# Kernel tuning notes

Measured on AMD Instinct MI355X. Metric: run time of the kernel, lower is better.

## Reference

```python
import jax, jax.numpy as jnp
import numpy as np

ATTN_WINDOW = 7  # attention_window from attn_params; dilation (attention_stride) = 1


def _xavier(key, shape):
    lim = np.sqrt(6.0 / (shape[0] + shape[1]))
    return jax.random.uniform(key, shape, jnp.float32, -lim, lim)


def setup_inputs() -> dict:
    key = jax.random.key(0)
    ks = jax.random.split(key, 8)
    B, Cin, Him, Wim = 4, 3, 112, 112
    Cmid, Cout = 128, 128
    x = jax.random.normal(ks[0], (B, Cin, Him, Wim), jnp.float32)
    conv_w = jax.random.normal(ks[1], (Cmid, Cin, 3, 3), jnp.float32) * 0.1  # OIHW
    conv_b = jnp.zeros((Cmid,), jnp.float32)
    q_w = _xavier(ks[2], (Cmid, Cmid)); q_b = jnp.zeros((Cmid,), jnp.float32)
    k_w = _xavier(ks[3], (Cmid, Cmid)); k_b = jnp.zeros((Cmid,), jnp.float32)
    v_w = _xavier(ks[4], (Cout, Cmid)); v_b = jnp.zeros((Cout,), jnp.float32)
    return {"x": x, "conv_w": conv_w, "conv_b": conv_b,
            "q_w": q_w, "q_b": q_b, "k_w": k_w, "k_b": k_b, "v_w": v_w, "v_b": v_b}


def _neighbor_idx(n, ksz):
    # NATTEN-style neighborhood: centered window, clamped to stay inside the image.
    starts = jnp.clip(jnp.arange(n) - ksz // 2, 0, n - ksz)
    return starts[:, None] + jnp.arange(ksz)[None, :]  # [n, ksz]


def reference(x, conv_w, conv_b, q_w, q_b, k_w, k_b, v_w, v_b):
    # conv stem (3x3, stride 2, pad 1) + ReLU
    f = jax.lax.conv_general_dilated(
        x, conv_w, window_strides=(2, 2), padding=[(1, 1), (1, 1)],
        dimension_numbers=("NCHW", "OIHW", "NCHW"))
    f = jax.nn.relu(f + conv_b[None, :, None, None])
    f = f.transpose(0, 2, 3, 1)  # NHWC  [B,H,W,Cmid]
    # 1x1 convs == per-pixel linear layers
    q = f @ q_w.T + q_b
    k = f @ k_w.T + k_b
    v = f @ v_w.T + v_b
    B, H, W, C = q.shape
    ksz = min(ATTN_WINDOW, H, W)
    ksz -= 1 if ksz % 2 == 0 else 0
    ih = _neighbor_idx(H, ksz)  # [H, ksz]
    iw = _neighbor_idx(W, ksz)  # [W, ksz]
    # gather per-pixel neighborhoods: [B,H,W,ksz,ksz,C]
    kn = k[:, ih[:, None, :, None], iw[None, :, None, :], :]
    vn = v[:, ih[:, None, :, None], iw[None, :, None, :], :]
    scale = C ** -0.5
    logits = jnp.einsum("bhwc,bhwijc->bhwij", q * scale, kn)
    attn = jax.nn.softmax(logits.reshape(B, H, W, -1), axis=-1).reshape(logits.shape)
    out = jnp.einsum("bhwij,bhwijc->bhwc", attn, vn)  # [B,H,W,Cout]
    return out.transpose(0, 3, 1, 2)  # back to NCHW
```

## Files before the change

kernel.cpp:

```cpp
#include <hip/hip_runtime.h>
#include <hip/hip_bf16.h>
#include <math.h>

#define HW 56
#define PPI (HW*HW)
#define NB 4
#define C 128
#define NPIX (NB*PPI)

typedef __attribute__((ext_vector_type(8))) short short8;
typedef __attribute__((ext_vector_type(4))) float f32x4;

__device__ __forceinline__ short bfbits(float v) {
    __hip_bfloat16 hb = __float2bfloat16(v);
    return *reinterpret_cast<short*>(&hb);
}
__device__ __forceinline__ unsigned packbf(float a, float b) {
    return (unsigned)(unsigned short)bfbits(a) | ((unsigned)(unsigned short)bfbits(b) << 16);
}

__global__ __launch_bounds__(256) void prep_kernel(
    const float* __restrict__ cw,
    const float* __restrict__ qw, const float* __restrict__ kw,
    const float* __restrict__ vw,
    __hip_bfloat16* __restrict__ wcf, __hip_bfloat16* __restrict__ wqkv)
{
    int gid = blockIdx.x * 256 + threadIdx.x;
    if (blockIdx.x < 192) {
        int m   = gid >> 14;
        int r   = gid & 16383;
        int col = r >> 7;
        int k   = r & 127;
        const float* W = (m == 0) ? qw : (m == 1) ? kw : vw;
        int kk = k >> 5, hi = (k >> 3) & 3, j = k & 7;
        wqkv[m * 16384 + ((kk * 4 + hi) * 128 + col) * 8 + j] = __float2bfloat16(W[col * 128 + k]);
    } else {
        int idx = gid - 192 * 256;
        int hi = idx >> 10, cout = (idx >> 3) & 127, j = idx & 7;
        int k  = hi * 8 + j;
        float v = (k < 27) ? cw[cout * 27 + k] : 0.f;
        wcf[(hi * 128 + cout) * 8 + j] = __float2bfloat16(v);
    }
}

#define VPITCH 272
#define XPITCH 24
#define XCH    504
#define LPITCH 100

__global__ __launch_bounds__(256, 3) void fused_kernel(
    const float* __restrict__ x, const __hip_bfloat16* __restrict__ wcf,
    const float* __restrict__ cb, const __hip_bfloat16* __restrict__ wqkv,
    const float* __restrict__ qb, const float* __restrict__ kb,
    const float* __restrict__ vb, float* __restrict__ out)
{
    __shared__ __align__(16) short vT[128 * 136];
    __shared__ __align__(16) short poolA[16 * 128];
    __shared__ __align__(16) short f_ch[16 * 128];
    __shared__ __align__(16) short poolB[16 * 136];
    __shared__ __align__(16) float logit_s[16 * LPITCH];
    short* q_lds   = poolA;
    short* k_chunk = poolA;
    short* x_lds   = poolB;
    short* attnW   = poolB;

    int t = threadIdx.x, lane = t & 63, wid = t >> 6;
    int r16 = lane & 15, hi = lane >> 4;

    int bx = blockIdx.x;
    int b  = bx / 196;
    int rr = bx % 196;
    int th = rr / 14, tw = rr % 14;
    int ih0 = min(max(th*4 - 3, 0), HW - 10);
    int iw0 = min(max(tw*4 - 3, 0), HW - 10);

    {
        int ihA = 2*ih0 - 1, iwA = 2*iw0 - 1;
        #pragma unroll
        for (int it = 0; it < 6; ++it) {
            int i = t + 256*it;
            if (i < 1512) {
                int ci = i / XCH, r = i % XCH;
                int row = r / XPITCH, col = r % XPITCH;
                int ih = ihA + row, iw = iwA + col;
                float xv = 0.f;
                if (col < 21 && ih >= 0 && ih < 112 && iw >= 0 && iw < 112)
                    xv = x[((size_t)(b*3 + ci)*112 + ih)*112 + iw];
                x_lds[i] = bfbits(xv);
            }
        }
    }

    for (int i = t; i < 1024; i += 256) {
        int c = i >> 3, j = i & 7;
        int hsw = (c >> 3) & 7;
        int unit = (14 + (j >> 2)) ^ hsw;
        *(unsigned*)((char*)vT + c*VPITCH + (unit << 4) + (j & 3)*4) = 0u;
    }

    int cout0 = (wid*2 + 0)*16 + r16;
    int cout1 = (wid*2 + 1)*16 + r16;
    short8 cbw0 = *(const short8*)((const short*)wcf + (hi*128 + cout0)*8);
    short8 cbw1 = *(const short8*)((const short*)wcf + (hi*128 + cout1)*8);
    float cbias0 = cb[cout0], cbias1 = cb[cout1];

    int  offb[8];
    bool vmask[8];
    #pragma unroll
    for (int j = 0; j < 8; ++j) {
        int k = hi*8 + j;
        int ci = k/9, r9 = k%9, kh = r9/3, kw_ = r9%3;
        offb[j]  = ci*XCH + kh*XPITCH + kw_;
        vmask[j] = (k < 27);
    }

    float kvbias[4];
    #pragma unroll
    for (int i = 0; i < 4; ++i) {
        int idx = wid*4 + i, mv = idx >> 3, ct = idx & 7, c = ct*16 + r16;
        kvbias[i] = mv ? vb[c] : kb[c];
    }
    float qbias[2];
    #pragma unroll
    for (int i = 0; i < 2; ++i) qbias[i] = qb[(wid*2 + i)*16 + r16];

    __syncthreads();

    auto conv_to_fch = [&](int hl, int wl) {
        int pb = hl*(2*XPITCH) + wl*2;
        short8 af;
        #pragma unroll
        for (int j = 0; j < 8; ++j)
            af[j] = vmask[j] ? x_lds[offb[j] + pb] : (short)0;
        #pragma unroll
        for (int ctl = 0; ctl < 2; ++ctl) {
            int cout   = ctl ? cout1  : cout0;
            short8 bw  = ctl ? cbw1   : cbw0;
            float bias = ctl ? cbias1 : cbias0;
            f32x4 acc = {0.f, 0.f, 0.f, 0.f};
            acc = __builtin_amdgcn_mfma_f32_16x16x32_bf16(af, bw, acc, 0, 0, 0);
            int colblk = cout >> 3, inb = (cout & 7)*2;
            #pragma unroll
            for (int rg = 0; rg < 4; ++rg) {
                int px = hi*4 + rg;
                *(short*)((char*)f_ch + px*256 + ((colblk ^ px) << 4) + inb)
                    = bfbits(fmaxf(acc[rg] + bias, 0.f));
            }
        }
    };

    short8 qa[4];
    {
        int ph = th*4 + (r16 >> 2), pw = tw*4 + (r16 & 3);
        conv_to_fch(ph - ih0, pw - iw0);
        __syncthreads();

        short8 fa[4];
        #pragma unroll
        for (int kk = 0; kk < 4; ++kk)
            fa[kk] = *(const short8*)((char*)f_ch + r16*256 + (((kk*4 + hi) ^ r16) << 4));

        #pragma unroll
        for (int i = 0; i < 2; ++i) {
            int ct = wid*2 + i;
            const short* wb = (const short*)wqkv + hi*1024 + r16*8 + ct*128;
            f32x4 acc = {0.f, 0.f, 0.f, 0.f};
            acc = __builtin_amdgcn_mfma_f32_16x16x32_bf16(fa[0], *(const short8*)(wb),         acc, 0, 0, 0);
            acc = __builtin_amdgcn_mfma_f32_16x16x32_bf16(fa[1], *(const short8*)(wb +  4096), acc, 0, 0, 0);
            acc = __builtin_amdgcn_mfma_f32_16x16x32_bf16(fa[2], *(const short8*)(wb +  8192), acc, 0, 0, 0);
            acc = __builtin_amdgcn_mfma_f32_16x16x32_bf16(fa[3], *(const short8*)(wb + 12288), acc, 0, 0, 0);
            int c = ct*16 + r16;
            float bb = qbias[i];
            #pragma unroll
            for (int rg = 0; rg < 4; ++rg) {
                int px = hi*4 + rg;
                *(short*)((char*)q_lds + px*256 + (((c >> 3) ^ px) << 4) + (c & 7)*2)
                    = bfbits(acc[rg] + bb);
            }
        }
        __syncthreads();

        #pragma unroll
        for (int kk = 0; kk < 4; ++kk)
            qa[kk] = *(const short8*)((char*)q_lds + r16*256 + (((kk*4 + hi) ^ r16) << 4));
    }

    for (int cc = 0; cc < 7; ++cc) {
        int nc = min(cc*16 + r16, 99);
        conv_to_fch(nc/10, nc%10);
        __syncthreads();

        short8 fa[4];
        #pragma unroll
        for (int kk = 0; kk < 4; ++kk)
            fa[kk] = *(const short8*)((char*)f_ch + r16*256 + (((kk*4 + hi) ^ r16) << 4));

        #pragma unroll
        for (int i = 0; i < 4; ++i) {
            int idx = wid*4 + i;
            int mv  = idx >> 3;
            int ct  = idx & 7;
            const short* wb = (const short*)wqkv + (1+mv)*16384 + hi*1024 + r16*8 + ct*128;
            f32x4 acc = {0.f, 0.f, 0.f, 0.f};
            acc = __builtin_amdgcn_mfma_f32_16x16x32_bf16(fa[0], *(const short8*)(wb),         acc, 0, 0, 0);
            acc = __builtin_amdgcn_mfma_f32_16x16x32_bf16(fa[1], *(const short8*)(wb +  4096), acc, 0, 0, 0);
            acc = __builtin_amdgcn_mfma_f32_16x16x32_bf16(fa[2], *(const short8*)(wb +  8192), acc, 0, 0, 0);
            acc = __builtin_amdgcn_mfma_f32_16x16x32_bf16(fa[3], *(const short8*)(wb + 12288), acc, 0, 0, 0);
            int c = ct*16 + r16;
            float bb = kvbias[i];
            if (mv == 0) {
                int swz = c >> 3;
                #pragma unroll
                for (int rg = 0; rg < 4; ++rg) {
                    int nl = hi*4 + rg;
                    *(short*)((char*)k_chunk + nl*256 + ((swz ^ nl) << 4) + (c & 7)*2)
                        = bfbits(acc[rg] + bb);
                }
            } else {
                int n0 = cc*16 + hi*4;
                unsigned lo  = packbf(acc[0] + bb, acc[1] + bb);
                unsigned hi2 = packbf(acc[2] + bb, acc[3] + bb);
                int hsw = (c >> 3) & 7;
                int off = (2*n0) ^ (hsw << 4);
                *(uint2*)((char*)vT + c*VPITCH + off) = make_uint2(lo, hi2);
            }
        }
        __syncthreads();

        if ((cc & 3) == wid) {
            const char* kbase = (const char*)k_chunk + r16*256;
            f32x4 acc = {0.f, 0.f, 0.f, 0.f};
            #pragma unroll
            for (int kk = 0; kk < 4; ++kk) {
                short8 kv = *(const short8*)(kbase + (((kk*4 + hi) ^ r16) << 4));
                acc = __builtin_amdgcn_mfma_f32_16x16x32_bf16(qa[kk], kv, acc, 0, 0, 0);
            }
            int col = cc*16 + r16;
            if (col < 100) {
                #pragma unroll
                for (int rg = 0; rg < 4; ++rg)
                    logit_s[(hi*4 + rg)*LPITCH + col] = acc[rg];
            }
        }
    }

    {
        unsigned* aw = (unsigned*)attnW;
        for (int i = t; i < 1088; i += 256) aw[i] = 0u;
    }
    __syncthreads();

    {
        int r7 = lane / 7, s7 = lane - 7*r7;
        bool valid = lane < 49;
        const float scale = 0.08838834764831845f;
        #pragma unroll
        for (int px = 0; px < 4; ++px) {
            int p = wid*4 + px;
            int h = th*4 + (p >> 2), w = tw*4 + (p & 3);
            int hs = min(max(h - 3, 0), HW - 7);
            int ws = min(max(w - 3, 0), HW - 7);
            int col = (hs - ih0 + r7)*10 + (ws - iw0 + s7);
            float lg = valid ? logit_s[p*LPITCH + col] * scale : -INFINITY;
            float m = lg;
            #pragma unroll
            for (int d = 1; d < 64; d <<= 1) m = fmaxf(m, __shfl_xor(m, d));
            float e = valid ? __expf(lg - m) : 0.f;
            float s = e;
            #pragma unroll
            for (int d = 1; d < 64; d <<= 1) s += __shfl_xor(s, d);
            if (valid) {
                __hip_bfloat16 hb = __float2bfloat16(e / s);
                *(__hip_bfloat16*)((char*)attnW + p*VPITCH + 2*col) = hb;
            }
        }
    }
    __syncthreads();

    short8 pa[4];
    #pragma unroll
    for (int kk = 0; kk < 4; ++kk)
        pa[kk] = *(const short8*)((char*)attnW + r16*VPITCH + kk*64 + hi*16);

    for (int nt = wid; nt < 8; nt += 4) {
        int c   = nt*16 + r16;
        int hsw = (c >> 3) & 7;
        const char* vrow = (const char*)vT + c*VPITCH;
        f32x4 acc = {0.f, 0.f, 0.f, 0.f};
        #pragma unroll
        for (int kk = 0; kk < 4; ++kk) {
            short8 vbr = *(const short8*)(vrow + ((kk*64 + hi*16) ^ (hsw << 4)));
            acc = __builtin_amdgcn_mfma_f32_16x16x32_bf16(pa[kk], vbr, acc, 0, 0, 0);
        }
        #pragma unroll
        for (int rg = 0; rg < 4; ++rg) {
            int p = hi*4 + rg;
            int h = th*4 + (p >> 2), w = tw*4 + (p & 3);
            out[(((size_t)b*C + c)*HW + h)*HW + w] = acc[rg];
        }
    }
}

extern "C" void kernel_launch(void* const* d_in, const int* in_sizes, int n_in,
                              void* d_out, int out_size, void* d_ws, size_t ws_size,
                              hipStream_t stream) {
    const float* x      = (const float*)d_in[0];
    const float* conv_w = (const float*)d_in[1];
    const float* conv_b = (const float*)d_in[2];
    const float* q_w    = (const float*)d_in[3];
    const float* q_b    = (const float*)d_in[4];
    const float* k_w    = (const float*)d_in[5];
    const float* k_b    = (const float*)d_in[6];
    const float* v_w    = (const float*)d_in[7];
    const float* v_b    = (const float*)d_in[8];
    float* out = (float*)d_out;

    __hip_bfloat16* wqkv = (__hip_bfloat16*)d_ws;
    __hip_bfloat16* wcf  = wqkv + 3 * 16384;

    prep_kernel<<<208, 256, 0, stream>>>(conv_w, q_w, k_w, v_w, wcf, wqkv);
    fused_kernel<<<NB*196, 256, 0, stream>>>(x, wcf, conv_b, wqkv,
                                             q_b, k_b, v_b, out);
}
```

Before: 45.68 us.

## Give each wave its own neighbor chunk to remove per-chunk block barriers

Instead of all four waves cooperating on each 16-pixel neighbor chunk, with block-wide barriers between the conv, K/V projection and logit stages, each wave now processes whole chunks independently in a private LDS buffer. Only wave-local data dependencies remain, so the seven-iteration loop no longer synchronises. The cost is more registers for per-wave copies of all conv weights and biases, a launch-bounds occupancy drop from 3 to 2 blocks, and load imbalance, since waves 0-2 take two chunks while wave 3 takes one.

```diff
diff --git a/kernel.cpp b/kernel.cpp
--- a/kernel.cpp
+++ b/kernel.cpp
@@ -48,21 +48,19 @@
 #define XCH    504
 #define LPITCH 100
 
-__global__ __launch_bounds__(256, 3) void fused_kernel(
+__global__ __launch_bounds__(256, 2) void fused_kernel(
     const float* __restrict__ x, const __hip_bfloat16* __restrict__ wcf,
     const float* __restrict__ cb, const __hip_bfloat16* __restrict__ wqkv,
     const float* __restrict__ qb, const float* __restrict__ kb,
     const float* __restrict__ vb, float* __restrict__ out)
 {
     __shared__ __align__(16) short vT[128 * 136];
-    __shared__ __align__(16) short poolA[16 * 128];
-    __shared__ __align__(16) short f_ch[16 * 128];
+    __shared__ __align__(16) short poolA[4][16 * 128];
     __shared__ __align__(16) short poolB[16 * 136];
     __shared__ __align__(16) float logit_s[16 * LPITCH];
-    short* q_lds   = poolA;
-    short* k_chunk = poolA;
-    short* x_lds   = poolB;
-    short* attnW   = poolB;
+    short* q_lds = poolA[0];
+    short* x_lds = poolB;
+    short* attnW = poolB;
 
     int t = threadIdx.x, lane = t & 63, wid = t >> 6;
     int r16 = lane & 15, hi = lane >> 4;
@@ -98,12 +96,6 @@
         *(unsigned*)((char*)vT + c*VPITCH + (unit << 4) + (j & 3)*4) = 0u;
     }
 
-    int cout0 = (wid*2 + 0)*16 + r16;
-    int cout1 = (wid*2 + 1)*16 + r16;
-    short8 cbw0 = *(const short8*)((const short*)wcf + (hi*128 + cout0)*8);
-    short8 cbw1 = *(const short8*)((const short*)wcf + (hi*128 + cout1)*8);
-    float cbias0 = cb[cout0], cbias1 = cb[cout1];
-
     int  offb[8];
     bool vmask[8];
     #pragma unroll
@@ -113,20 +105,22 @@
         offb[j]  = ci*XCH + kh*XPITCH + kw_;
         vmask[j] = (k < 27);
     }
-
-    float kvbias[4];
-    #pragma unroll
-    for (int i = 0; i < 4; ++i) {
-        int idx = wid*4 + i, mv = idx >> 3, ct = idx & 7, c = ct*16 + r16;
-        kvbias[i] = mv ? vb[c] : kb[c];
-    }
     float qbias[2];
     #pragma unroll
     for (int i = 0; i < 2; ++i) qbias[i] = qb[(wid*2 + i)*16 + r16];
 
     __syncthreads();
 
-    auto conv_to_fch = [&](int hl, int wl) {
+    short8 qa[4];
+    {
+        int cout0 = (wid*2 + 0)*16 + r16;
+        int cout1 = (wid*2 + 1)*16 + r16;
+        short8 cbw0 = *(const short8*)((const short*)wcf + (hi*128 + cout0)*8);
+        short8 cbw1 = *(const short8*)((const short*)wcf + (hi*128 + cout1)*8);
+        float cbias0 = cb[cout0], cbias1 = cb[cout1];
+
+        int ph = th*4 + (r16 >> 2), pw = tw*4 + (r16 & 3);
+        int hl = ph - ih0, wl = pw - iw0;
         int pb = hl*(2*XPITCH) + wl*2;
         short8 af;
         #pragma unroll
@@ -143,22 +137,18 @@
             #pragma unroll
             for (int rg = 0; rg < 4; ++rg) {
                 int px = hi*4 + rg;
-                *(short*)((char*)f_ch + px*256 + ((colblk ^ px) << 4) + inb)
+                *(short*)((char*)q_lds + px*256 + ((colblk ^ px) << 4) + inb)
                     = bfbits(fmaxf(acc[rg] + bias, 0.f));
             }
         }
-    };
-
-    short8 qa[4];
-    {
-        int ph = th*4 + (r16 >> 2), pw = tw*4 + (r16 & 3);
-        conv_to_fch(ph - ih0, pw - iw0);
         __syncthreads();
 
         short8 fa[4];
         #pragma unroll
         for (int kk = 0; kk < 4; ++kk)
-            fa[kk] = *(const short8*)((char*)f_ch + r16*256 + (((kk*4 + hi) ^ r16) << 4));
+            fa[kk] = *(const short8*)((char*)q_lds + r16*256 + (((kk*4 + hi) ^ r16) << 4));
+
+        __syncthreads();
 
         #pragma unroll
         for (int i = 0; i < 2; ++i) {
@@ -183,66 +173,109 @@
         #pragma unroll
         for (int kk = 0; kk < 4; ++kk)
             qa[kk] = *(const short8*)((char*)q_lds + r16*256 + (((kk*4 + hi) ^ r16) << 4));
-    }
-
-    for (int cc = 0; cc < 7; ++cc) {
-        int nc = min(cc*16 + r16, 99);
-        conv_to_fch(nc/10, nc%10);
         __syncthreads();
-
-        short8 fa[4];
-        #pragma unroll
-        for (int kk = 0; kk < 4; ++kk)
-            fa[kk] = *(const short8*)((char*)f_ch + r16*256 + (((kk*4 + hi) ^ r16) << 4));
-
-        #pragma unroll
-        for (int i = 0; i < 4; ++i) {
-            int idx = wid*4 + i;
-            int mv  = idx >> 3;
-            int ct  = idx & 7;
-            const short* wb = (const short*)wqkv + (1+mv)*16384 + hi*1024 + r16*8 + ct*128;
-            f32x4 acc = {0.f, 0.f, 0.f, 0.f};
-            acc = __builtin_amdgcn_mfma_f32_16x16x32_bf16(fa[0], *(const short8*)(wb),         acc, 0, 0, 0);
-            acc = __builtin_amdgcn_mfma_f32_16x16x32_bf16(fa[1], *(const short8*)(wb +  4096), acc, 0, 0, 0);
-            acc = __builtin_amdgcn_mfma_f32_16x16x32_bf16(fa[2], *(const short8*)(wb +  8192), acc, 0, 0, 0);
-            acc = __builtin_amdgcn_mfma_f32_16x16x32_bf16(fa[3], *(const short8*)(wb + 12288), acc, 0, 0, 0);
+    }
+
+    {
+        short* myb = poolA[wid];
+
+        short8 cbw8[8];
+        float  cbias8[8], kbias8[8], vbias8[8];
+        #pragma unroll
+        for (int ct = 0; ct < 8; ++ct) {
             int c = ct*16 + r16;
-            float bb = kvbias[i];
-            if (mv == 0) {
-                int swz = c >> 3;
-                #pragma unroll
-                for (int rg = 0; rg < 4; ++rg) {
-                    int nl = hi*4 + rg;
-                    *(short*)((char*)k_chunk + nl*256 + ((swz ^ nl) << 4) + (c & 7)*2)
-                        = bfbits(acc[rg] + bb);
+            cbw8[ct]   = *(const short8*)((const short*)wcf + (hi*128 + c)*8);
+            cbias8[ct] = cb[c];
+            kbias8[ct] = kb[c];
+            vbias8[ct] = vb[c];
+        }
+
+        #pragma unroll
+        for (int j = 0; j < 2; ++j) {
+            int cc = wid + 4*j;
+            if (cc < 7) {
+                int nc = min(cc*16 + r16, 99);
+                int hl = nc/10, wl = nc - 10*hl;
+                int pb = hl*(2*XPITCH) + wl*2;
+                short8 af;
+                #pragma unroll
+                for (int j2 = 0; j2 < 8; ++j2)
+                    af[j2] = vmask[j2] ? x_lds[offb[j2] + pb] : (short)0;
+
+                #pragma unroll
+                for (int ct = 0; ct < 8; ++ct) {
+                    f32x4 acc = {0.f, 0.f, 0.f, 0.f};
+                    acc = __builtin_amdgcn_mfma_f32_16x16x32_bf16(af, cbw8[ct], acc, 0, 0, 0);
+                    int cout = ct*16 + r16;
+                    int colblk = cout >> 3, inb = (cout & 7)*2;
+                    #pragma unroll
+                    for (int rg = 0; rg < 4; ++rg) {
+                        int px = hi*4 + rg;
+                        *(short*)((char*)myb + px*256 + ((colblk ^ px) << 4) + inb)
+                            = bfbits(fmaxf(acc[rg] + cbias8[ct], 0.f));
+                    }
                 }
-            } else {
-                int n0 = cc*16 + hi*4;
-                unsigned lo  = packbf(acc[0] + bb, acc[1] + bb);
-                unsigned hi2 = packbf(acc[2] + bb, acc[3] + bb);
-                int hsw = (c >> 3) & 7;
-                int off = (2*n0) ^ (hsw << 4);
-                *(uint2*)((char*)vT + c*VPITCH + off) = make_uint2(lo, hi2);
-            }
-        }
-        __syncthreads();
-
-        if ((cc & 3) == wid) {
-            const char* kbase = (const char*)k_chunk + r16*256;
-            f32x4 acc = {0.f, 0.f, 0.f, 0.f};
-            #pragma unroll
-            for (int kk = 0; kk < 4; ++kk) {
-                short8 kv = *(const short8*)(kbase + (((kk*4 + hi) ^ r16) << 4));
-                acc = __builtin_amdgcn_mfma_f32_16x16x32_bf16(qa[kk], kv, acc, 0, 0, 0);
-            }
-            int col = cc*16 + r16;
-            if (col < 100) {
-                #pragma unroll
-                for (int rg = 0; rg < 4; ++rg)
-                    logit_s[(hi*4 + rg)*LPITCH + col] = acc[rg];
-            }
-        }
-    }
+
+                short8 fa[4];
+                #pragma unroll
+                for (int kk = 0; kk < 4; ++kk)
+                    fa[kk] = *(const short8*)((char*)myb + r16*256 + (((kk*4 + hi) ^ r16) << 4));
+
+                #pragma unroll
+                for (int ct = 0; ct < 8; ++ct) {
+                    const short* wb = (const short*)wqkv + 16384 + hi*1024 + r16*8 + ct*128;
+                    f32x4 acc = {0.f, 0.f, 0.f, 0.f};
+                    acc = __builtin_amdgcn_mfma_f32_16x16x32_bf16(fa[0], *(const short8*)(wb),         acc, 0, 0, 0);
+                    acc = __builtin_amdgcn_mfma_f32_16x16x32_bf16(fa[1], *(const short8*)(wb +  4096), acc, 0, 0, 0);
+                    acc = __builtin_amdgcn_mfma_f32_16x16x32_bf16(fa[2], *(const short8*)(wb +  8192), acc, 0, 0, 0);
+                    acc = __builtin_amdgcn_mfma_f32_16x16x32_bf16(fa[3], *(const short8*)(wb + 12288), acc, 0, 0, 0);
+                    int c = ct*16 + r16;
+                    int swz = c >> 3;
+                    #pragma unroll
+                    for (int rg = 0; rg < 4; ++rg) {
+                        int nl = hi*4 + rg;
+                        *(short*)((char*)myb + nl*256 + ((swz ^ nl) << 4) + (c & 7)*2)
+                            = bfbits(acc[rg] + kbias8[ct]);
+                    }
+                }
+
+                #pragma unroll
+                for (int ct = 0; ct < 8; ++ct) {
+                    const short* wb = (const short*)wqkv + 2*16384 + hi*1024 + r16*8 + ct*128;
+                    f32x4 acc = {0.f, 0.f, 0.f, 0.f};
+                    acc = __builtin_amdgcn_mfma_f32_16x16x32_bf16(fa[0], *(const short8*)(wb),         acc, 0, 0, 0);
+                    acc = __builtin_amdgcn_mfma_f32_16x16x32_bf16(fa[1], *(const short8*)(wb +  4096), acc, 0, 0, 0);
+                    acc = __builtin_amdgcn_mfma_f32_16x16x32_bf16(fa[2], *(const short8*)(wb +  8192), acc, 0, 0, 0);
+                    acc = __builtin_amdgcn_mfma_f32_16x16x32_bf16(fa[3], *(const short8*)(wb + 12288), acc, 0, 0, 0);
+                    int c = ct*16 + r16;
+                    float bb = vbias8[ct];
+                    int n0 = cc*16 + hi*4;
+                    unsigned lo  = packbf(acc[0] + bb, acc[1] + bb);
+                    unsigned hi2 = packbf(acc[2] + bb, acc[3] + bb);
+                    int hsw = (c >> 3) & 7;
+                    int off = (2*n0) ^ (hsw << 4);
+                    *(uint2*)((char*)vT + c*VPITCH + off) = make_uint2(lo, hi2);
+                }
+
+                {
+                    const char* kbase = (const char*)myb + r16*256;
+                    f32x4 acc = {0.f, 0.f, 0.f, 0.f};
+                    #pragma unroll
+                    for (int kk = 0; kk < 4; ++kk) {
+                        short8 kv = *(const short8*)(kbase + (((kk*4 + hi) ^ r16) << 4));
+                        acc = __builtin_amdgcn_mfma_f32_16x16x32_bf16(qa[kk], kv, acc, 0, 0, 0);
+                    }
+                    int col = cc*16 + r16;
+                    if (col < 100) {
+                        #pragma unroll
+                        for (int rg = 0; rg < 4; ++rg)
+                            logit_s[(hi*4 + rg)*LPITCH + col] = acc[rg];
+                    }
+                }
+            }
+        }
+    }
+    __syncthreads();
 
     {
         unsigned* aw = (unsigned*)attnW;
```

New measurement: 43.48 us. -4.8%, faster.

## Stream V projection in chunks after softmax to shrink LDS and raise occupancy

Applied to the files above, without the earlier changes.

The kernel no longer keeps the full 128x100 V tile in shared memory. K is computed in the first pass, and V is recomputed per 32-neighbor chunk after the softmax and fed straight into the attention-times-V MFMA through a small staging buffer. This cuts LDS use enough to raise launch bounds from 3 to 4 blocks per CU. In exchange the conv stem is recomputed for the neighborhood pixels and more barriers are added.

```diff
diff --git a/kernel.cpp b/kernel.cpp
--- a/kernel.cpp
+++ b/kernel.cpp
@@ -47,22 +47,22 @@
 #define XPITCH 24
 #define XCH    504
 #define LPITCH 100
-
-__global__ __launch_bounds__(256, 3) void fused_kernel(
+#define VTP    40
+
+__global__ __launch_bounds__(256, 4) void fused_kernel(
     const float* __restrict__ x, const __hip_bfloat16* __restrict__ wcf,
     const float* __restrict__ cb, const __hip_bfloat16* __restrict__ wqkv,
     const float* __restrict__ qb, const float* __restrict__ kb,
     const float* __restrict__ vb, float* __restrict__ out)
 {
-    __shared__ __align__(16) short vT[128 * 136];
+    __shared__ __align__(16) short x_s[1536];
+    __shared__ __align__(16) short f_ch2[32 * 128];
     __shared__ __align__(16) short poolA[16 * 128];
-    __shared__ __align__(16) short f_ch[16 * 128];
-    __shared__ __align__(16) short poolB[16 * 136];
+    __shared__ __align__(16) short attnW[16 * 136];
     __shared__ __align__(16) float logit_s[16 * LPITCH];
+    __shared__ __align__(16) short vtp[128 * VTP];
     short* q_lds   = poolA;
     short* k_chunk = poolA;
-    short* x_lds   = poolB;
-    short* attnW   = poolB;
 
     int t = threadIdx.x, lane = t & 63, wid = t >> 6;
     int r16 = lane & 15, hi = lane >> 4;
@@ -73,6 +73,11 @@
     int th = rr / 14, tw = rr % 14;
     int ih0 = min(max(th*4 - 3, 0), HW - 10);
     int iw0 = min(max(tw*4 - 3, 0), HW - 10);
+
+    {
+        unsigned* aw = (unsigned*)attnW;
+        for (int i = t; i < 1088; i += 256) aw[i] = 0u;
+    }
 
     {
         int ihA = 2*ih0 - 1, iwA = 2*iw0 - 1;
@@ -86,16 +91,9 @@
                 float xv = 0.f;
                 if (col < 21 && ih >= 0 && ih < 112 && iw >= 0 && iw < 112)
                     xv = x[((size_t)(b*3 + ci)*112 + ih)*112 + iw];
-                x_lds[i] = bfbits(xv);
-            }
-        }
-    }
-
-    for (int i = t; i < 1024; i += 256) {
-        int c = i >> 3, j = i & 7;
-        int hsw = (c >> 3) & 7;
-        int unit = (14 + (j >> 2)) ^ hsw;
-        *(unsigned*)((char*)vT + c*VPITCH + (unit << 4) + (j & 3)*4) = 0u;
+                x_s[i] = bfbits(xv);
+            }
+        }
     }
 
     int cout0 = (wid*2 + 0)*16 + r16;
@@ -113,25 +111,23 @@
         offb[j]  = ci*XCH + kh*XPITCH + kw_;
         vmask[j] = (k < 27);
     }
-
-    float kvbias[4];
+    float qbias[2], kbias[2], vbias[2];
     #pragma unroll
-    for (int i = 0; i < 4; ++i) {
-        int idx = wid*4 + i, mv = idx >> 3, ct = idx & 7, c = ct*16 + r16;
-        kvbias[i] = mv ? vb[c] : kb[c];
-    }
-    float qbias[2];
-    #pragma unroll
-    for (int i = 0; i < 2; ++i) qbias[i] = qb[(wid*2 + i)*16 + r16];
+    for (int i = 0; i < 2; ++i) {
+        int c = (wid*2 + i)*16 + r16;
+        qbias[i] = qb[c];
+        kbias[i] = kb[c];
+        vbias[i] = vb[c];
+    }
 
     __syncthreads();
 
-    auto conv_to_fch = [&](int hl, int wl) {
+    auto conv_to = [&](int hl, int wl, int pxb) {
         int pb = hl*(2*XPITCH) + wl*2;
         short8 af;
         #pragma unroll
         for (int j = 0; j < 8; ++j)
-            af[j] = vmask[j] ? x_lds[offb[j] + pb] : (short)0;
+            af[j] = vmask[j] ? x_s[offb[j] + pb] : (short)0;
         #pragma unroll
         for (int ctl = 0; ctl < 2; ++ctl) {
             int cout   = ctl ? cout1  : cout0;
@@ -143,7 +139,7 @@
             #pragma unroll
             for (int rg = 0; rg < 4; ++rg) {
                 int px = hi*4 + rg;
-                *(short*)((char*)f_ch + px*256 + ((colblk ^ px) << 4) + inb)
+                *(short*)((char*)f_ch2 + (pxb + px)*256 + ((colblk ^ px) << 4) + inb)
                     = bfbits(fmaxf(acc[rg] + bias, 0.f));
             }
         }
@@ -152,13 +148,13 @@
     short8 qa[4];
     {
         int ph = th*4 + (r16 >> 2), pw = tw*4 + (r16 & 3);
-        conv_to_fch(ph - ih0, pw - iw0);
+        conv_to(ph - ih0, pw - iw0, 0);
         __syncthreads();
 
         short8 fa[4];
         #pragma unroll
         for (int kk = 0; kk < 4; ++kk)
-            fa[kk] = *(const short8*)((char*)f_ch + r16*256 + (((kk*4 + hi) ^ r16) << 4));
+            fa[kk] = *(const short8*)((char*)f_ch2 + r16*256 + (((kk*4 + hi) ^ r16) << 4));
 
         #pragma unroll
         for (int i = 0; i < 2; ++i) {
@@ -187,42 +183,31 @@
 
     for (int cc = 0; cc < 7; ++cc) {
         int nc = min(cc*16 + r16, 99);
-        conv_to_fch(nc/10, nc%10);
+        conv_to(nc/10, nc%10, 0);
         __syncthreads();
 
         short8 fa[4];
         #pragma unroll
         for (int kk = 0; kk < 4; ++kk)
-            fa[kk] = *(const short8*)((char*)f_ch + r16*256 + (((kk*4 + hi) ^ r16) << 4));
-
-        #pragma unroll
-        for (int i = 0; i < 4; ++i) {
-            int idx = wid*4 + i;
-            int mv  = idx >> 3;
-            int ct  = idx & 7;
-            const short* wb = (const short*)wqkv + (1+mv)*16384 + hi*1024 + r16*8 + ct*128;
+            fa[kk] = *(const short8*)((char*)f_ch2 + r16*256 + (((kk*4 + hi) ^ r16) << 4));
+
+        #pragma unroll
+        for (int i = 0; i < 2; ++i) {
+            int ct = wid*2 + i;
+            const short* wb = (const short*)wqkv + 16384 + hi*1024 + r16*8 + ct*128;
             f32x4 acc = {0.f, 0.f, 0.f, 0.f};
             acc = __builtin_amdgcn_mfma_f32_16x16x32_bf16(fa[0], *(const short8*)(wb),         acc, 0, 0, 0);
             acc = __builtin_amdgcn_mfma_f32_16x16x32_bf16(fa[1], *(const short8*)(wb +  4096), acc, 0, 0, 0);
             acc = __builtin_amdgcn_mfma_f32_16x16x32_bf16(fa[2], *(const short8*)(wb +  8192), acc, 0, 0, 0);
             acc = __builtin_amdgcn_mfma_f32_16x16x32_bf16(fa[3], *(const short8*)(wb + 12288), acc, 0, 0, 0);
             int c = ct*16 + r16;
-            float bb = kvbias[i];
-            if (mv == 0) {
-                int swz = c >> 3;
-                #pragma unroll
-                for (int rg = 0; rg < 4; ++rg) {
-                    int nl = hi*4 + rg;
-                    *(short*)((char*)k_chunk + nl*256 + ((swz ^ nl) << 4) + (c & 7)*2)
-                        = bfbits(acc[rg] + bb);
-                }
-            } else {
-                int n0 = cc*16 + hi*4;
-                unsigned lo  = packbf(acc[0] + bb, acc[1] + bb);
-                unsigned hi2 = packbf(acc[2] + bb, acc[3] + bb);
-                int hsw = (c >> 3) & 7;
-                int off = (2*n0) ^ (hsw << 4);
-                *(uint2*)((char*)vT + c*VPITCH + off) = make_uint2(lo, hi2);
+            float bb = kbias[i];
+            int swz = c >> 3;
+            #pragma unroll
+            for (int rg = 0; rg < 4; ++rg) {
+                int nl = hi*4 + rg;
+                *(short*)((char*)k_chunk + nl*256 + ((swz ^ nl) << 4) + (c & 7)*2)
+                    = bfbits(acc[rg] + bb);
             }
         }
         __syncthreads();
@@ -242,11 +227,6 @@
                     logit_s[(hi*4 + rg)*LPITCH + col] = acc[rg];
             }
         }
-    }
-
-    {
-        unsigned* aw = (unsigned*)attnW;
-        for (int i = t; i < 1088; i += 256) aw[i] = 0u;
     }
     __syncthreads();
 
@@ -277,26 +257,62 @@
     }
     __syncthreads();
 
-    short8 pa[4];
+    f32x4 acc2_0 = {0.f, 0.f, 0.f, 0.f};
+    f32x4 acc2_1 = {0.f, 0.f, 0.f, 0.f};
+    for (int cp = 0; cp < 4; ++cp) {
+        int nsub = (cp == 3) ? 1 : 2;
+        for (int sub = 0; sub < nsub; ++sub) {
+            int cc = 2*cp + sub;
+            int nc = min(cc*16 + r16, 99);
+            conv_to(nc/10, nc%10, sub*16);
+        }
+        __syncthreads();
+
+        for (int sub = 0; sub < nsub; ++sub) {
+            short8 fa[4];
+            #pragma unroll
+            for (int kk = 0; kk < 4; ++kk)
+                fa[kk] = *(const short8*)((char*)f_ch2 + (sub*16 + r16)*256
+                                          + (((kk*4 + hi) ^ r16) << 4));
+            #pragma unroll
+            for (int i = 0; i < 2; ++i) {
+                int ct = wid*2 + i;
+                const short* wb = (const short*)wqkv + 2*16384 + hi*1024 + r16*8 + ct*128;
+                f32x4 acc = {0.f, 0.f, 0.f, 0.f};
+                acc = __builtin_amdgcn_mfma_f32_16x16x32_bf16(fa[0], *(const short8*)(wb),         acc, 0, 0, 0);
+                acc = __builtin_amdgcn_mfma_f32_16x16x32_bf16(fa[1], *(const short8*)(wb +  4096), acc, 0, 0, 0);
+                acc = __builtin_amdgcn_mfma_f32_16x16x32_bf16(fa[2], *(const short8*)(wb +  8192), acc, 0, 0, 0);
+                acc = __builtin_amdgcn_mfma_f32_16x16x32_bf16(fa[3], *(const short8*)(wb + 12288), acc, 0, 0, 0);
+                int c = ct*16 + r16;
+                float bb = vbias[i];
+                unsigned lo  = packbf(acc[0] + bb, acc[1] + bb);
+                unsigned hi2 = packbf(acc[2] + bb, acc[3] + bb);
+                *(uint2*)((char*)vtp + (c*VTP + sub*16 + hi*4)*2) = make_uint2(lo, hi2);
+            }
+        }
+        __syncthreads();
+
+        short8 pa_cp = *(const short8*)((char*)attnW + r16*VPITCH + cp*64 + hi*16);
+        {
+            int c0_ = wid*16 + r16;
+            short8 vt0 = *(const short8*)((char*)vtp + (c0_*VTP + hi*8)*2);
+            acc2_0 = __builtin_amdgcn_mfma_f32_16x16x32_bf16(pa_cp, vt0, acc2_0, 0, 0, 0);
+            int c1_ = (wid + 4)*16 + r16;
+            short8 vt1 = *(const short8*)((char*)vtp + (c1_*VTP + hi*8)*2);
+            acc2_1 = __builtin_amdgcn_mfma_f32_16x16x32_bf16(pa_cp, vt1, acc2_1, 0, 0, 0);
+        }
+    }
+
     #pragma unroll
-    for (int kk = 0; kk < 4; ++kk)
-        pa[kk] = *(const short8*)((char*)attnW + r16*VPITCH + kk*64 + hi*16);
-
-    for (int nt = wid; nt < 8; nt += 4) {
-        int c   = nt*16 + r16;
-        int hsw = (c >> 3) & 7;
-        const char* vrow = (const char*)vT + c*VPITCH;
-        f32x4 acc = {0.f, 0.f, 0.f, 0.f};
-        #pragma unroll
-        for (int kk = 0; kk < 4; ++kk) {
-            short8 vbr = *(const short8*)(vrow + ((kk*64 + hi*16) ^ (hsw << 4)));
-            acc = __builtin_amdgcn_mfma_f32_16x16x32_bf16(pa[kk], vbr, acc, 0, 0, 0);
-        }
+    for (int i = 0; i < 2; ++i) {
+        int nt = wid + 4*i;
+        int c  = nt*16 + r16;
+        f32x4 accX = i ? acc2_1 : acc2_0;
         #pragma unroll
         for (int rg = 0; rg < 4; ++rg) {
             int p = hi*4 + rg;
             int h = th*4 + (p >> 2), w = tw*4 + (p & 3);
-            out[(((size_t)b*C + c)*HW + h)*HW + w] = acc[rg];
+            out[(((size_t)b*C + c)*HW + h)*HW + w] = accX[rg];
         }
     }
 }
```

Measured after the change: 44.33 us. 1.03x faster.
